# Performance work log

Measured on AMD Instinct MI355X. Metric: run time of the kernel, lower is better.

## Reference

```python
import math
import jax, jax.numpy as jnp
from jax import lax
import numpy as np

LN_EPS = 1e-5
K = 3          # deform-conv kernel size
PAD = 1        # 'same' padding so offset map matches output resolution


def setup_inputs() -> dict:
    key = jax.random.key(0)
    ks = jax.random.split(key, 6)
    B, C, H, W, Co = 4, 256, 64, 64, 256
    x = jax.random.normal(ks[0], (B, C, H, W), jnp.float32)
    dwc_w = jax.random.normal(ks[1], (C, 1, K, K), jnp.float32) * 0.02
    ln_w = jnp.ones((C,), jnp.float32)
    ln_b = jnp.zeros((C,), jnp.float32)
    fcd_w = jax.random.normal(ks[2], (1, C, 1, 1), jnp.float32) * 0.02
    fca_w = jax.random.normal(ks[3], (1, C, 1, 1), jnp.float32) * 0.02
    fan_in = C * K * K
    dconv_w = jax.random.normal(ks[4], (Co, C, K, K), jnp.float32) / math.sqrt(fan_in)
    dconv_b = jnp.zeros((Co,), jnp.float32)
    return dict(x=x, dwc_w=dwc_w, ln_w=ln_w, ln_b=ln_b,
                fcd_w=fcd_w, fca_w=fca_w, dconv_w=dconv_w, dconv_b=dconv_b)


def _bilinear_sample(x, py, px):
    # x: [B,C,H,W]; py/px: [B,KK,H,W] float sample positions (zero-padded border)
    B, C, H, W = x.shape
    y0 = jnp.floor(py); x0 = jnp.floor(px)
    y1 = y0 + 1.0;      x1 = x0 + 1.0
    wy1 = py - y0; wy0 = 1.0 - wy1
    wx1 = px - x0; wx0 = 1.0 - wx1

    def gather(yy, xx):
        valid = ((yy >= 0) & (yy < H) & (xx >= 0) & (xx < W)).astype(x.dtype)
        iy = jnp.clip(yy, 0, H - 1).astype(jnp.int32)
        ix = jnp.clip(xx, 0, W - 1).astype(jnp.int32)
        # per-batch fancy gather -> [B,C,KK,H,W]
        v = jax.vmap(lambda img, a, b: img[:, a, b])(x, iy, ix)
        return v * valid[:, None]

    return (gather(y0, x0) * (wy0 * wx0)[:, None]
          + gather(y0, x1) * (wy0 * wx1)[:, None]
          + gather(y1, x0) * (wy1 * wx0)[:, None]
          + gather(y1, x1) * (wy1 * wx1)[:, None])


def reference(x, dwc_w, ln_w, ln_b, fcd_w, fca_w, dconv_w, dconv_b):
    B, C, H, W = x.shape
    KK = K * K
    # --- offset branch ---
    h = lax.conv_general_dilated(x, dwc_w, (1, 1), ((1, 1), (1, 1)),
                                 dimension_numbers=('NCHW', 'OIHW', 'NCHW'),
                                 feature_group_count=C)
    mu = h.mean(axis=1, keepdims=True)
    var = h.var(axis=1, keepdims=True)
    h = (h - mu) * lax.rsqrt(var + LN_EPS)
    h = h * ln_w[None, :, None, None] + ln_b[None, :, None, None]
    h = jax.nn.relu(h)
    r = jax.nn.relu(jnp.einsum('bchw,oc->bohw', h, fcd_w[:, :, 0, 0]))      # [B,1,H,W]
    t = jnp.einsum('bchw,oc->bohw', h, fca_w[:, :, 0, 0])
    theta = (t / (1.0 + jnp.abs(t))) * (math.pi / 180.0)                     # softsign * pi/180
    ox = r * jnp.cos(theta)
    oy = r * jnp.sin(theta)
    # torch code: offsets = cat([ox tiled KK, oy tiled KK], dim=1) -> [B,2KK,H,W]
    off = jnp.concatenate([jnp.tile(ox, (1, KK, 1, 1)), jnp.tile(oy, (1, KK, 1, 1))], axis=1)
    # torchvision DeformConv2d convention: channel 2k = dy, channel 2k+1 = dx
    dy = off[:, 0::2]   # [B,KK,H,W]
    dx = off[:, 1::2]
    # --- deformable sampling ---
    ky = jnp.repeat(jnp.arange(K), K).astype(x.dtype)   # kernel row per tap
    kx = jnp.tile(jnp.arange(K), K).astype(x.dtype)     # kernel col per tap
    py = (jnp.arange(H, dtype=x.dtype) - PAD)[None, None, :, None] + ky[None, :, None, None] + dy
    px = (jnp.arange(W, dtype=x.dtype) - PAD)[None, None, None, :] + kx[None, :, None, None] + dx
    sampled = _bilinear_sample(x, py, px)               # [B,C,KK,H,W]
    Co = dconv_w.shape[0]
    out = jnp.einsum('bckhw,ock->bohw', sampled, dconv_w.reshape(Co, C, KK))
    return out + dconv_b[None, :, None, None]
```

## Files before the change

### kernel.cpp

```cpp
#include <hip/hip_runtime.h>
#include <hip/hip_bf16.h>

#define B_   4
#define C_   256
#define CO_  256
#define H_   64
#define W_   64
#define HW_  4096

typedef __attribute__((ext_vector_type(8))) short short8;
typedef __attribute__((ext_vector_type(4))) float f32x4;
typedef __attribute__((ext_vector_type(2))) float f32x2;

static __device__ __forceinline__ unsigned short f2bf(float f) {
    unsigned u = __builtin_bit_cast(unsigned, f);
    unsigned r = (u + 0x7fffu + ((u >> 16) & 1u)) >> 16;
    return (unsigned short)r;
}
static __device__ __forceinline__ f32x2 pk_mul(f32x2 a, f32x2 b) {
    f32x2 d; asm("v_pk_mul_f32 %0, %1, %2" : "=v"(d) : "v"(a), "v"(b)); return d;
}
static __device__ __forceinline__ f32x2 pk_fma(f32x2 a, f32x2 b, f32x2 c) {
    f32x2 d; asm("v_pk_fma_f32 %0, %1, %2, %3" : "=v"(d) : "v"(a), "v"(b), "v"(c)); return d;
}
static __device__ __forceinline__ f32x2 pk_add(f32x2 a, f32x2 b) {
    f32x2 d; asm("v_pk_add_f32 %0, %1, %2" : "=v"(d) : "v"(a), "v"(b)); return d;
}
static __device__ __forceinline__ unsigned cvtpk(float a, float b) {
    unsigned r; asm("v_cvt_pk_bf16_f32 %0, %1, %2" : "=v"(r) : "v"(a), "v"(b)); return r;
}
static __device__ __forceinline__ f32x2 unpack_bf2(unsigned d) {
    f32x2 v;
    v.x = __builtin_bit_cast(float, d << 16);
    v.y = __builtin_bit_cast(float, d & 0xffff0000u);
    return v;
}

__global__ void k_pre(const float* __restrict__ x, unsigned short* __restrict__ xT,
                      const float* __restrict__ w, unsigned short* __restrict__ Bt,
                      const float* __restrict__ dwc_w, float* __restrict__ dwcT)
{
    int bid = blockIdx.x;
    int tid = threadIdx.x;
    if (bid < 1024) {
        __shared__ float t[32][132];
        int b   = bid >> 8;
        int rem = bid & 255;
        int hwT = rem >> 1, cT = rem & 1;
        int hw0 = hwT * 32, c0 = cT * 128;
        const float* src = x + (size_t)b * C_ * HW_;
        {
            int hw4 = (tid & 7) << 2;
            int cr  = tid >> 3;
#pragma unroll
            for (int it = 0; it < 4; ++it) {
                int c = cr + it * 32;
                f32x4 v = *(const f32x4*)(src + (size_t)(c0 + c) * HW_ + hw0 + hw4);
                t[hw4 + 0][c] = v.x;
                t[hw4 + 1][c] = v.y;
                t[hw4 + 2][c] = v.z;
                t[hw4 + 3][c] = v.w;
            }
        }
        __syncthreads();
        {
            int c8  = (tid & 15) << 3;
            int hwr = tid >> 4;
            unsigned short* dst = xT + (size_t)(((b << 12) + hw0) * 256) + c0 + c8;
#pragma unroll
            for (int it = 0; it < 2; ++it) {
                int hw = hwr + it * 16;
                f32x4 va = *(const f32x4*)&t[hw][c8];
                f32x4 vb = *(const f32x4*)&t[hw][c8 + 4];
                uint4 u;
                u.x = cvtpk(va.x, va.y);
                u.y = cvtpk(va.z, va.w);
                u.z = cvtpk(vb.x, vb.y);
                u.w = cvtpk(vb.z, vb.w);
                *(uint4*)(dst + (size_t)hw * 256) = u;
            }
        }
    } else {
        int pb = bid - 1024;
        if (pb < 9) dwcT[pb * 256 + tid] = dwc_w[tid * 9 + pb];
        int e = pb * 256 + tid;
        int j   = e & 7;
        int l4  = (e >> 3) & 3;
        int l15 = (e >> 5) & 15;
        int ks  = (e >> 9) & 7;
        int og  = (e >> 12) & 15;
        int k   = e >> 16;
        int o = og * 16 + l15;
        int c = ks * 32 + l4 * 8 + j;
        Bt[e] = f2bf(w[(o * C_ + c) * 9 + k]);
    }
}

__global__ void k_offsets(const unsigned short* __restrict__ xT,
                          const float* __restrict__ dwcT,
                          const float* __restrict__ ln_w,
                          const float* __restrict__ ln_b,
                          const float* __restrict__ fcd_w,
                          const float* __restrict__ fca_w,
                          float* __restrict__ OX, float* __restrict__ OY)
{
    int tid = threadIdx.x;
    int bi = blockIdx.x;
    int g = ((bi & 7) << 6) | (bi >> 3);
    int p0 = g << 5;
    int b = p0 >> 12;
    int y = (p0 >> 6) & 63;
    int xh = p0 & 63;
    int gpos = tid >> 4;
    int csub = tid & 15;
    int ch0 = csub << 4;
    const unsigned short* xb = xT + (size_t)b * HW_ * C_;

    f32x2 acc2[8];
#pragma unroll
    for (int i = 0; i < 8; ++i) { acc2[i].x = 0.f; acc2[i].y = 0.f; }
#pragma unroll
    for (int j = 0; j < 9; ++j) {
        int gy = y + j / 3 - 1, gx = xh + gpos + j % 3 - 1;
        if (gy >= 0 && gy < H_ && gx >= 0 && gx < W_) {
            const unsigned short* p = xb + (size_t)((gy << 6) + gx) * 256 + ch0;
            short8 rlo = *(const short8*)(p);
            short8 rhi = *(const short8*)(p + 8);
            const float* wrow = dwcT + j * 256 + ch0;
#pragma unroll
            for (int q = 0; q < 4; ++q) {
                f32x4 wv = *(const f32x4*)(wrow + q * 4);
                f32x2 w01v; w01v.x = wv.x; w01v.y = wv.y;
                f32x2 w23v; w23v.x = wv.z; w23v.y = wv.w;
                unsigned lo = (q < 2) ? ((unsigned*)&rlo)[q * 2] : ((unsigned*)&rhi)[(q - 2) * 2];
                unsigned hi = (q < 2) ? ((unsigned*)&rlo)[q * 2 + 1] : ((unsigned*)&rhi)[(q - 2) * 2 + 1];
                acc2[q * 2 + 0] = pk_fma(unpack_bf2(lo), w01v, acc2[q * 2 + 0]);
                acc2[q * 2 + 1] = pk_fma(unpack_bf2(hi), w23v, acc2[q * 2 + 1]);
            }
        }
    }
    f32x2 sum2, sq2;
    sum2.x = 0.f; sum2.y = 0.f; sq2.x = 0.f; sq2.y = 0.f;
#pragma unroll
    for (int i = 0; i < 8; ++i) {
        sum2 = pk_add(sum2, acc2[i]);
        sq2  = pk_fma(acc2[i], acc2[i], sq2);
    }
    float s1 = sum2.x + sum2.y, s2 = sq2.x + sq2.y;
#pragma unroll
    for (int m = 1; m <= 8; m <<= 1) {
        s1 += __shfl_xor(s1, m);
        s2 += __shfl_xor(s2, m);
    }
    float mu  = s1 * (1.f / 256.f);
    float var = s2 * (1.f / 256.f) - mu * mu;
    float rs  = rsqrtf(var + 1e-5f);
    float d1 = 0.f, d2 = 0.f;
#pragma unroll
    for (int q = 0; q < 4; ++q) {
        f32x4 lwv = *(const f32x4*)(ln_w  + ch0 + q * 4);
        f32x4 lbv = *(const f32x4*)(ln_b  + ch0 + q * 4);
        f32x4 fdv = *(const f32x4*)(fcd_w + ch0 + q * 4);
        f32x4 fav = *(const f32x4*)(fca_w + ch0 + q * 4);
#pragma unroll
        for (int i = 0; i < 4; ++i) {
            float av = (i & 1) ? acc2[q * 2 + (i >> 1)].y : acc2[q * 2 + (i >> 1)].x;
            float hn = (av - mu) * rs * lwv[i] + lbv[i];
            hn = fmaxf(hn, 0.f);
            d1 = fmaf(hn, fdv[i], d1);
            d2 = fmaf(hn, fav[i], d2);
        }
    }
#pragma unroll
    for (int m = 1; m <= 8; m <<= 1) {
        d1 += __shfl_xor(d1, m);
        d2 += __shfl_xor(d2, m);
    }
    if (csub == 0) {
        float r0 = fmaxf(d1, 0.f);
        float theta = d2 / (1.f + fabsf(d2)) * 0.017453292519943295f;
        int pos = p0 + gpos;
        OX[pos] = r0 * cosf(theta);
        OY[pos] = r0 * sinf(theta);
    }
}

__launch_bounds__(256, 4)
__global__ void k_main(const unsigned short* __restrict__ xT,
                       const float* __restrict__ OX, const float* __restrict__ OY,
                       const unsigned short* __restrict__ Bt,
                       const float* __restrict__ bias,
                       float* __restrict__ out)
{
    __shared__ __align__(16) unsigned char smem[32768];

    int tid = threadIdx.x;
    int bi = blockIdx.x;
    int g = ((bi & 7) << 7) | (bi >> 3);
    int tile = g >> 1;
    int n0g = g & 1;
    int p0 = tile << 5;
    int b = p0 >> 12;
    int y = (p0 >> 6) & 63;
    int xh = p0 & 63;

    int lane = tid & 63, wid = tid >> 6;
    int l15 = lane & 15, l4 = lane >> 4;

    f32x4 acc[2][2];
#pragma unroll
    for (int m = 0; m < 2; ++m)
#pragma unroll
        for (int n = 0; n < 2; ++n) {
            acc[m][n].x = 0.f; acc[m][n].y = 0.f; acc[m][n].z = 0.f; acc[m][n].w = 0.f;
        }

    int gpos = tid >> 3;
    unsigned csub = (unsigned)tid & 7u;
    const char* xbB = (const char*)(xT + (size_t)b * HW_ * C_);
    const unsigned short* bwave = Bt + (unsigned)(n0g * 8 + wid * 2) * 4096u
                                     + (unsigned)(l15 * 32 + l4 * 8);
    unsigned rowb = (unsigned)gpos * 512u;
    float ox = OX[p0 + gpos], oy = OY[p0 + gpos];

    unsigned o00, o01, o10, o11;
    f32x2 W00, W01, W10, W11;

#define GADDR(k)                                                                  \
    {   int ky = (k) / 3, kx = (k) - ky * 3;                                      \
        float dyv = ((k) <= 4) ? ox : oy;                                         \
        float dxv = ((k) <= 3) ? ox : oy;                                         \
        float py = (float)(y - 1 + ky) + dyv;                                     \
        float px = (float)(xh + gpos - 1 + kx) + dxv;                             \
        float y0f = floorf(py), x0f = floorf(px);                                 \
        int y0 = (int)y0f, x0 = (int)x0f;                                         \
        int y1 = y0 + 1, x1 = x0 + 1;                                             \
        float wy1 = py - y0f, wy0 = 1.f - wy1;                                    \
        float wx1 = px - x0f, wx0 = 1.f - wx1;                                    \
        float vy0 = (y0 >= 0 && y0 < H_) ? 1.f : 0.f;                             \
        float vy1 = (y1 >= 0 && y1 < H_) ? 1.f : 0.f;                             \
        float vx0 = (x0 >= 0 && x0 < W_) ? 1.f : 0.f;                             \
        float vx1 = (x1 >= 0 && x1 < W_) ? 1.f : 0.f;                             \
        float w00 = wy0 * wx0 * vy0 * vx0, w01 = wy0 * wx1 * vy0 * vx1;           \
        float w10 = wy1 * wx0 * vy1 * vx0, w11 = wy1 * wx1 * vy1 * vx1;           \
        W00.x = w00; W00.y = w00; W01.x = w01; W01.y = w01;                       \
        W10.x = w10; W10.y = w10; W11.x = w11; W11.y = w11;                       \
        int y0c = min(max(y0, 0), H_ - 1), y1c = min(max(y1, 0), H_ - 1);         \
        int x0c = min(max(x0, 0), W_ - 1), x1c = min(max(x1, 0), W_ - 1);         \
        unsigned cb = csub << 4;                                                  \
        o00 = (unsigned)((y0c << 6) + x0c) * 512u + cb;                           \
        o01 = (unsigned)((y0c << 6) + x1c) * 512u + cb;                           \
        o10 = (unsigned)((y1c << 6) + x0c) * 512u + cb;                           \
        o11 = (unsigned)((y1c << 6) + x1c) * 512u + cb;                           \
    }

#define GATHER_TAP(hbase)                                                         \
    {   _Pragma("unroll")                                                         \
        for (int cq = 0; cq < 4; ++cq) {                                          \
            unsigned gb = (unsigned)cq * 128u;                                    \
            short8 r00 = *(const short8*)(xbB + o00 + gb);                        \
            short8 r01 = *(const short8*)(xbB + o01 + gb);                        \
            short8 r10 = *(const short8*)(xbB + o10 + gb);                        \
            short8 r11 = *(const short8*)(xbB + o11 + gb);                        \
            uint4 pkv;                                                            \
            _Pragma("unroll")                                                     \
            for (int dw = 0; dw < 4; ++dw) {                                      \
                f32x2 a2 = pk_mul(unpack_bf2(((unsigned*)&r00)[dw]), W00);        \
                a2 = pk_fma(unpack_bf2(((unsigned*)&r01)[dw]), W01, a2);          \
                a2 = pk_fma(unpack_bf2(((unsigned*)&r10)[dw]), W10, a2);          \
                a2 = pk_fma(unpack_bf2(((unsigned*)&r11)[dw]), W11, a2);          \
                ((unsigned*)&pkv)[dw] = cvtpk(a2.x, a2.y);                        \
            }                                                                     \
            unsigned slot = ((unsigned)cq * 8u + csub) ^ ((unsigned)gpos & 7u);   \
            *(uint4*)(smem + (hbase) + rowb + slot * 16u) = pkv;                  \
        }                                                                         \
    }

#define MFMA_TAP(k, hbase)                                                        \
    {   const unsigned short* bk = bwave + (unsigned)(k) * 65536u;                \
        _Pragma("unroll")                                                         \
        for (int ks = 0; ks < 8; ++ks) {                                          \
            short8 bf0 = *(const short8*)(bk + ks * 512);                         \
            short8 bf1 = *(const short8*)(bk + 4096 + ks * 512);                  \
            unsigned sl = ((unsigned)(ks * 4 + l4) ^ ((unsigned)l15 & 7u)) << 4;  \
            short8 a0 = *(const short8*)(smem + (hbase) + (unsigned)l15 * 512u + sl);        \
            short8 a1 = *(const short8*)(smem + (hbase) + (unsigned)(16 + l15) * 512u + sl); \
            acc[0][0] = __builtin_amdgcn_mfma_f32_16x16x32_bf16(a0, bf0, acc[0][0], 0, 0, 0); \
            acc[0][1] = __builtin_amdgcn_mfma_f32_16x16x32_bf16(a0, bf1, acc[0][1], 0, 0, 0); \
            acc[1][0] = __builtin_amdgcn_mfma_f32_16x16x32_bf16(a1, bf0, acc[1][0], 0, 0, 0); \
            acc[1][1] = __builtin_amdgcn_mfma_f32_16x16x32_bf16(a1, bf1, acc[1][1], 0, 0, 0); \
        }                                                                         \
    }

    GADDR(0);
    GATHER_TAP(0u);
    __syncthreads();

#pragma unroll
    for (int k = 0; k < 9; ++k) {
        unsigned cur = (k & 1) ? 16384u : 0u;
        unsigned nxt = (k & 1) ? 0u : 16384u;
        if (k < 8) {
            GADDR(k + 1);
            GATHER_TAP(nxt);
        }
        MFMA_TAP(k, cur);
        __syncthreads();
    }

#pragma unroll
    for (int nf = 0; nf < 2; ++nf) {
        int col = n0g * 128 + wid * 32 + nf * 16 + l15;
        float bv = bias[col];
        float* obase = out + ((size_t)(b * CO_ + col)) * HW_ + (y << 6) + xh;
#pragma unroll
        for (int mf = 0; mf < 2; ++mf) {
            f32x4 v;
            v.x = acc[mf][nf].x + bv;
            v.y = acc[mf][nf].y + bv;
            v.z = acc[mf][nf].z + bv;
            v.w = acc[mf][nf].w + bv;
            *(f32x4*)(obase + mf * 16 + l4 * 4) = v;
        }
    }
}

extern "C" void kernel_launch(void* const* d_in, const int* in_sizes, int n_in,
                              void* d_out, int out_size, void* d_ws, size_t ws_size,
                              hipStream_t stream) {
    const float* x      = (const float*)d_in[0];
    const float* dwc_w  = (const float*)d_in[1];
    const float* ln_w   = (const float*)d_in[2];
    const float* ln_b   = (const float*)d_in[3];
    const float* fcd_w  = (const float*)d_in[4];
    const float* fca_w  = (const float*)d_in[5];
    const float* dconv_w= (const float*)d_in[6];
    const float* dconv_b= (const float*)d_in[7];
    float* out = (float*)d_out;

    unsigned char* ws = (unsigned char*)d_ws;
    unsigned short* xT = (unsigned short*)(ws);
    unsigned short* Bt = (unsigned short*)(ws + 8388608);
    float* dwcT        = (float*)(ws + 9568256);
    float* OX          = (float*)(ws + 9577472);
    float* OY          = (float*)(ws + 9643008);

    k_pre<<<3328, 256, 0, stream>>>(x, xT, dconv_w, Bt, dwc_w, dwcT);
    k_offsets<<<512, 512, 0, stream>>>(xT, dwcT, ln_w, ln_b, fcd_w, fca_w, OX, OY);
    k_main<<<1024, 256, 0, stream>>>(xT, OX, OY, Bt, dconv_b, out);
}
```

Baseline: 82.84 us.

## Warp-specialize deform-conv main kernel into gather producers and MFMA consumers

Splits each 512-thread block into four producer waves that compute bilinear gathers into shared memory and four consumer waves that run the MFMA GEMM from the double buffer. The tile grows from 32 to 64 pixels (a full row) per block, so each B fragment load now feeds four M fragments. The intent is to overlap gather latency with matrix math and improve B reuse. In exchange, each wave does only half the work, shared memory doubles to 64KB, and occupancy per CU drops.

```diff
diff --git a/kernel.cpp b/kernel.cpp
--- a/kernel.cpp
+++ b/kernel.cpp
@@ -185,43 +185,34 @@
     }
 }
 
-__launch_bounds__(256, 4)
+__launch_bounds__(512, 4)
 __global__ void k_main(const unsigned short* __restrict__ xT,
                        const float* __restrict__ OX, const float* __restrict__ OY,
                        const unsigned short* __restrict__ Bt,
                        const float* __restrict__ bias,
                        float* __restrict__ out)
 {
-    __shared__ __align__(16) unsigned char smem[32768];
+    __shared__ __align__(16) unsigned char smem[65536];
 
     int tid = threadIdx.x;
     int bi = blockIdx.x;
-    int g = ((bi & 7) << 7) | (bi >> 3);
+    int g = ((bi & 7) << 6) | (bi >> 3);
     int tile = g >> 1;
     int n0g = g & 1;
-    int p0 = tile << 5;
-    int b = p0 >> 12;
-    int y = (p0 >> 6) & 63;
-    int xh = p0 & 63;
+    int b = tile >> 6;
+    int y = tile & 63;
 
     int lane = tid & 63, wid = tid >> 6;
     int l15 = lane & 15, l4 = lane >> 4;
-
-    f32x4 acc[2][2];
-#pragma unroll
-    for (int m = 0; m < 2; ++m)
-#pragma unroll
-        for (int n = 0; n < 2; ++n) {
-            acc[m][n].x = 0.f; acc[m][n].y = 0.f; acc[m][n].z = 0.f; acc[m][n].w = 0.f;
-        }
-
-    int gpos = tid >> 3;
-    unsigned csub = (unsigned)tid & 7u;
+    bool producer = (wid < 4);
+
+    int gpos = tid >> 2;
+    unsigned qc = (unsigned)tid & 3u;
     const char* xbB = (const char*)(xT + (size_t)b * HW_ * C_);
-    const unsigned short* bwave = Bt + (unsigned)(n0g * 8 + wid * 2) * 4096u
-                                     + (unsigned)(l15 * 32 + l4 * 8);
-    unsigned rowb = (unsigned)gpos * 512u;
-    float ox = OX[p0 + gpos], oy = OY[p0 + gpos];
+    float ox = 0.f, oy = 0.f;
+    if (producer) { ox = OX[(tile << 6) + gpos]; oy = OY[(tile << 6) + gpos]; }
+    unsigned pwbase = (unsigned)gpos * 512u + qc * 128u;
+    unsigned pswz = ((unsigned)gpos & 7u);
 
     unsigned o00, o01, o10, o11;
     f32x2 W00, W01, W10, W11;
@@ -231,7 +222,7 @@
         float dyv = ((k) <= 4) ? ox : oy;                                         \
         float dxv = ((k) <= 3) ? ox : oy;                                         \
         float py = (float)(y - 1 + ky) + dyv;                                     \
-        float px = (float)(xh + gpos - 1 + kx) + dxv;                             \
+        float px = (float)(gpos - 1 + kx) + dxv;                                  \
         float y0f = floorf(py), x0f = floorf(px);                                 \
         int y0 = (int)y0f, x0 = (int)x0f;                                         \
         int y1 = y0 + 1, x1 = x0 + 1;                                             \
@@ -247,17 +238,16 @@
         W10.x = w10; W10.y = w10; W11.x = w11; W11.y = w11;                       \
         int y0c = min(max(y0, 0), H_ - 1), y1c = min(max(y1, 0), H_ - 1);         \
         int x0c = min(max(x0, 0), W_ - 1), x1c = min(max(x1, 0), W_ - 1);         \
-        unsigned cb = csub << 4;                                                  \
-        o00 = (unsigned)((y0c << 6) + x0c) * 512u + cb;                           \
-        o01 = (unsigned)((y0c << 6) + x1c) * 512u + cb;                           \
-        o10 = (unsigned)((y1c << 6) + x0c) * 512u + cb;                           \
-        o11 = (unsigned)((y1c << 6) + x1c) * 512u + cb;                           \
+        o00 = (unsigned)((y0c << 6) + x0c) * 512u + qc * 128u;                    \
+        o01 = (unsigned)((y0c << 6) + x1c) * 512u + qc * 128u;                    \
+        o10 = (unsigned)((y1c << 6) + x0c) * 512u + qc * 128u;                    \
+        o11 = (unsigned)((y1c << 6) + x1c) * 512u + qc * 128u;                    \
     }
 
 #define GATHER_TAP(hbase)                                                         \
     {   _Pragma("unroll")                                                         \
-        for (int cq = 0; cq < 4; ++cq) {                                          \
-            unsigned gb = (unsigned)cq * 128u;                                    \
+        for (int j = 0; j < 8; ++j) {                                             \
+            unsigned gb = (unsigned)j * 16u;                                      \
             short8 r00 = *(const short8*)(xbB + o00 + gb);                        \
             short8 r01 = *(const short8*)(xbB + o01 + gb);                        \
             short8 r10 = *(const short8*)(xbB + o10 + gb);                        \
@@ -271,10 +261,20 @@
                 a2 = pk_fma(unpack_bf2(((unsigned*)&r11)[dw]), W11, a2);          \
                 ((unsigned*)&pkv)[dw] = cvtpk(a2.x, a2.y);                        \
             }                                                                     \
-            unsigned slot = ((unsigned)cq * 8u + csub) ^ ((unsigned)gpos & 7u);   \
-            *(uint4*)(smem + (hbase) + rowb + slot * 16u) = pkv;                  \
+            *(uint4*)(smem + (hbase) + pwbase + (((unsigned)j ^ pswz) * 16u)) = pkv; \
         }                                                                         \
     }
+
+    int cwid = wid - 4;
+    f32x4 acc[4][2];
+#pragma unroll
+    for (int m = 0; m < 4; ++m)
+#pragma unroll
+        for (int n = 0; n < 2; ++n) {
+            acc[m][n].x = 0.f; acc[m][n].y = 0.f; acc[m][n].z = 0.f; acc[m][n].w = 0.f;
+        }
+    const unsigned short* bwave = Bt + (unsigned)(n0g * 8 + (cwid < 0 ? 0 : cwid) * 2) * 4096u
+                                     + (unsigned)(l15 * 32 + l4 * 8);
 
 #define MFMA_TAP(k, hbase)                                                        \
     {   const unsigned short* bk = bwave + (unsigned)(k) * 65536u;                \
@@ -282,45 +282,55 @@
         for (int ks = 0; ks < 8; ++ks) {                                          \
             short8 bf0 = *(const short8*)(bk + ks * 512);                         \
             short8 bf1 = *(const short8*)(bk + 4096 + ks * 512);                  \
-            unsigned sl = ((unsigned)(ks * 4 + l4) ^ ((unsigned)l15 & 7u)) << 4;  \
-            short8 a0 = *(const short8*)(smem + (hbase) + (unsigned)l15 * 512u + sl);        \
-            short8 a1 = *(const short8*)(smem + (hbase) + (unsigned)(16 + l15) * 512u + sl); \
-            acc[0][0] = __builtin_amdgcn_mfma_f32_16x16x32_bf16(a0, bf0, acc[0][0], 0, 0, 0); \
-            acc[0][1] = __builtin_amdgcn_mfma_f32_16x16x32_bf16(a0, bf1, acc[0][1], 0, 0, 0); \
-            acc[1][0] = __builtin_amdgcn_mfma_f32_16x16x32_bf16(a1, bf0, acc[1][0], 0, 0, 0); \
-            acc[1][1] = __builtin_amdgcn_mfma_f32_16x16x32_bf16(a1, bf1, acc[1][1], 0, 0, 0); \
+            unsigned sl = ((unsigned)(ks >> 1)) * 128u +                          \
+                          ((((unsigned)(ks & 1) * 4u + (unsigned)l4) ^           \
+                            ((unsigned)l15 & 7u)) * 16u);                         \
+            _Pragma("unroll")                                                     \
+            for (int mf = 0; mf < 4; ++mf) {                                      \
+                unsigned row = (unsigned)(mf * 16 + l15);                         \
+                short8 a = *(const short8*)(smem + (hbase) + row * 512u + sl);    \
+                acc[mf][0] = __builtin_amdgcn_mfma_f32_16x16x32_bf16(a, bf0, acc[mf][0], 0, 0, 0); \
+                acc[mf][1] = __builtin_amdgcn_mfma_f32_16x16x32_bf16(a, bf1, acc[mf][1], 0, 0, 0); \
+            }                                                                     \
         }                                                                         \
     }
 
-    GADDR(0);
-    GATHER_TAP(0u);
+    if (producer) {
+        GADDR(0);
+        GATHER_TAP(0u);
+    }
     __syncthreads();
 
 #pragma unroll
     for (int k = 0; k < 9; ++k) {
-        unsigned cur = (k & 1) ? 16384u : 0u;
-        unsigned nxt = (k & 1) ? 0u : 16384u;
-        if (k < 8) {
-            GADDR(k + 1);
-            GATHER_TAP(nxt);
-        }
-        MFMA_TAP(k, cur);
+        unsigned cur = (k & 1) ? 32768u : 0u;
+        unsigned nxt = (k & 1) ? 0u : 32768u;
+        if (producer) {
+            if (k < 8) {
+                GADDR(k + 1);
+                GATHER_TAP(nxt);
+            }
+        } else {
+            MFMA_TAP(k, cur);
+        }
         __syncthreads();
     }
 
-#pragma unroll
-    for (int nf = 0; nf < 2; ++nf) {
-        int col = n0g * 128 + wid * 32 + nf * 16 + l15;
-        float bv = bias[col];
-        float* obase = out + ((size_t)(b * CO_ + col)) * HW_ + (y << 6) + xh;
-#pragma unroll
-        for (int mf = 0; mf < 2; ++mf) {
-            f32x4 v;
-            v.x = acc[mf][nf].x + bv;
-            v.y = acc[mf][nf].y + bv;
-            v.z = acc[mf][nf].z + bv;
-            v.w = acc[mf][nf].w + bv;
-            *(f32x4*)(obase + mf * 16 + l4 * 4) = v;
+    if (!producer) {
+#pragma unroll
+        for (int nf = 0; nf < 2; ++nf) {
+            int col = n0g * 128 + cwid * 32 + nf * 16 + l15;
+            float bv = bias[col];
+            float* obase = out + ((size_t)(b * CO_ + col)) * HW_ + (y << 6);
+#pragma unroll
+            for (int mf = 0; mf < 4; ++mf) {
+                f32x4 v;
+                v.x = acc[mf][nf].x + bv;
+                v.y = acc[mf][nf].y + bv;
+                v.z = acc[mf][nf].z + bv;
+                v.w = acc[mf][nf].w + bv;
+                *(f32x4*)(obase + mf * 16 + l4 * 4) = v;
+            }
         }
     }
 }
@@ -347,5 +357,5 @@
 
     k_pre<<<3328, 256, 0, stream>>>(x, xT, dconv_w, Bt, dwc_w, dwcT);
     k_offsets<<<512, 512, 0, stream>>>(xT, dwcT, ln_w, ln_b, fcd_w, fca_w, OX, OY);
-    k_main<<<1024, 256, 0, stream>>>(xT, OX, OY, Bt, dconv_b, out);
-}
+    k_main<<<512, 512, 0, stream>>>(xT, OX, OY, Bt, dconv_b, out);
+}
```

New measurement: 138.6 us. 67.3% more time.
